# Performance work log

Measured on AMD Instinct MI355X. Metric: run time of the kernel, lower is better.

## Reference

```python
import jax, jax.numpy as jnp
import numpy as np

NPOINT = 2048
RADIUS = 0.1
NSAMPLE = 32


def fps(xyz, npoint):
    # Furthest point sampling, deterministic start at index 0 (matches pointnet2_utils).
    B, N, _ = xyz.shape
    dist0 = jnp.full((B, N), 1e10, dtype=xyz.dtype)
    far0 = jnp.zeros((B,), dtype=jnp.int32)

    def step(carry, _):
        dist, far = carry
        centroid = jnp.take_along_axis(xyz, far[:, None, None], axis=1)  # (B,1,3)
        d = jnp.sum((xyz - centroid) ** 2, axis=-1)                      # (B,N)
        dist = jnp.minimum(dist, d)
        new_far = jnp.argmax(dist, axis=-1).astype(jnp.int32)
        return (dist, new_far), far

    _, idx = jax.lax.scan(step, (dist0, far0), None, length=npoint)
    return idx.T  # (B, npoint)


def ball_query(xyz, new_xyz, radius, nsample):
    # For each center, indices of up to nsample points within radius (pad with first hit).
    N = xyz.shape[1]
    sqr = jnp.sum((new_xyz[:, :, None, :] - xyz[:, None, :, :]) ** 2, axis=-1)  # (B,S,N)
    cand = jnp.where(sqr <= radius * radius, jnp.arange(N, dtype=jnp.int32), N)
    cand = jnp.sort(cand, axis=-1)[:, :, :nsample]  # (B,S,K)
    first = cand[:, :, :1]
    first = jnp.where(first == N, 0, first)
    return jnp.where(cand == N, first, cand)


def batched_gather(points, idx):
    # points (B,N,C), idx (B,...) -> (B,...,C)
    return jax.vmap(lambda p, i: p[i])(points, idx)


def reference(xyz, features, W0, b0, W1, b1, W2, b2):
    # xyz: (B,N,3), features: (B,C,N)
    fps_idx = fps(xyz, NPOINT)                                  # (B,S)
    new_xyz = batched_gather(xyz, fps_idx)                      # (B,S,3)
    idx = ball_query(xyz, new_xyz, RADIUS, NSAMPLE)             # (B,S,K)

    grouped_xyz = batched_gather(xyz, idx) - new_xyz[:, :, None, :]   # (B,S,K,3) relative coords
    grouped_feat = batched_gather(features.transpose(0, 2, 1), idx)   # (B,S,K,C)
    grouped = jnp.concatenate([grouped_xyz, grouped_feat], axis=-1)   # (B,S,K,C+3)
    x = grouped.transpose(0, 3, 1, 2)                                 # (B,C+3,S,K)

    # SharedMLP: 1x1 conv2d + ReLU stack
    x = jax.nn.relu(jnp.einsum('oi,bisk->bosk', W0, x) + b0[None, :, None, None])
    x = jax.nn.relu(jnp.einsum('oi,bisk->bosk', W1, x) + b1[None, :, None, None])
    x = jax.nn.relu(jnp.einsum('oi,bisk->bosk', W2, x) + b2[None, :, None, None])

    new_features = jnp.max(x, axis=-1)  # max-pool over nsample -> (B,128,S)
    return new_xyz, new_features


def setup_inputs() -> dict:
    key = jax.random.key(0)
    ks = jax.random.split(key, 8)
    B, N, C = 4, 8192, 64
    s = 0.05  # keep activations in a sane range through 3 relu layers
    return {
        'xyz': jax.random.uniform(ks[0], (B, N, 3), dtype=jnp.float32),
        'features': jax.random.normal(ks[1], (B, C, N), dtype=jnp.float32),
        'W0': jax.random.normal(ks[2], (64, 67), dtype=jnp.float32) * s,
        'b0': jax.random.normal(ks[3], (64,), dtype=jnp.float32) * s,
        'W1': jax.random.normal(ks[4], (64, 64), dtype=jnp.float32) * s,
        'b1': jax.random.normal(ks[5], (64,), dtype=jnp.float32) * s,
        'W2': jax.random.normal(ks[6], (128, 64), dtype=jnp.float32) * s,
        'b2': jax.random.normal(ks[7], (128,), dtype=jnp.float32) * s,
    }
```

## Files before the change

kernel.cpp:

```cpp
#include <hip/hip_runtime.h>

#define NB 4
#define NPTS 8192
#define NPOINT 2048
#define NSAMPLE 32
#define CF 64
#define CIN 67
#define G 8

typedef float f32x2 __attribute__((ext_vector_type(2)));
typedef unsigned long long u64;

__device__ __forceinline__ f32x2 pk_add(f32x2 a, f32x2 b) {
  f32x2 d;
  asm("v_pk_add_f32 %0, %1, %2" : "=v"(d) : "v"(a), "v"(b));
  return d;
}
__device__ __forceinline__ f32x2 pk_mul(f32x2 a, f32x2 b) {
  f32x2 d;
  asm("v_pk_mul_f32 %0, %1, %2" : "=v"(d) : "v"(a), "v"(b));
  return d;
}

template <int CTRL, int RM>
__device__ __forceinline__ int dppi(int v) {
  return __builtin_amdgcn_update_dpp(0, v, CTRL, RM, 0xf, true);
}
template <int CTRL, int RM>
__device__ __forceinline__ u64 kstep(u64 k) {
  unsigned lo = (unsigned)k, hi = (unsigned)(k >> 32);
  unsigned olo = (unsigned)dppi<CTRL, RM>((int)lo);
  unsigned ohi = (unsigned)dppi<CTRL, RM>((int)hi);
  u64 o = ((u64)ohi << 32) | olo;
  return o > k ? o : k;
}

__global__ __launch_bounds__(512) void fps_kernel(const float* __restrict__ xyz,
                                                  float* __restrict__ new_xyz) {
  const int b = blockIdx.x;
  const int tid = threadIdx.x;
  __shared__ float sx[NPTS], sy[NPTS], sz[NPTS];
  __shared__ __align__(16) float cbuf[NPOINT * 3];
  __shared__ __align__(16) u64 skey[2][8];
  const float* xb = xyz + (size_t)b * NPTS * 3;
  for (int i = tid; i < NPTS; i += 512) {
    sx[i] = xb[3 * i + 0];
    sy[i] = xb[3 * i + 1];
    sz[i] = xb[3 * i + 2];
  }
  __syncthreads();
  f32x2 px[8], py[8], pz[8];
  float dist[16];
#pragma unroll
  for (int j = 0; j < 8; ++j) {
    int p0 = tid + (2 * j) * 512, p1 = tid + (2 * j + 1) * 512;
    px[j].x = sx[p0]; px[j].y = sx[p1];
    py[j].x = sy[p0]; py[j].y = sy[p1];
    pz[j].x = sz[p0]; pz[j].y = sz[p1];
    dist[2 * j] = 1e10f; dist[2 * j + 1] = 1e10f;
  }
  const int lane = tid & 63;
  const int wid = tid >> 6;
  int far = 0;
  for (int it = 0; it < NPOINT; ++it) {
    const float cx = sx[far], cy = sy[far], cz = sz[far];
    if (tid == 0) {
      cbuf[it * 3 + 0] = cx; cbuf[it * 3 + 1] = cy; cbuf[it * 3 + 2] = cz;
    }
    f32x2 ncx, ncy, ncz;
    ncx.x = -cx; ncx.y = -cx;
    ncy.x = -cy; ncy.y = -cy;
    ncz.x = -cz; ncz.y = -cz;
    float tb = -1.0f;
    int br = 0;
#pragma unroll
    for (int j = 0; j < 8; ++j) {
      f32x2 dx = pk_add(px[j], ncx);
      f32x2 dy = pk_add(py[j], ncy);
      f32x2 dz = pk_add(pz[j], ncz);
      f32x2 xx = pk_mul(dx, dx);
      f32x2 yy = pk_mul(dy, dy);
      f32x2 dd = pk_add(pk_add(xx, yy), pk_mul(dz, dz));
      float n0 = fminf(dist[2 * j], dd.x);
      float n1 = fminf(dist[2 * j + 1], dd.y);
      dist[2 * j] = n0; dist[2 * j + 1] = n1;
      bool g0 = n0 > tb; tb = g0 ? n0 : tb; br = g0 ? (2 * j) : br;
      bool g1 = n1 > tb; tb = g1 ? n1 : tb; br = g1 ? (2 * j + 1) : br;
    }
    u64 key = ((u64)__float_as_uint(tb) << 32) |
              (unsigned)~(unsigned)(tid + (br << 9));
    key = kstep<0x111, 0xf>(key);
    key = kstep<0x112, 0xf>(key);
    key = kstep<0x114, 0xf>(key);
    key = kstep<0x118, 0xf>(key);
    key = kstep<0x142, 0xa>(key);
    key = kstep<0x143, 0xc>(key);
    const int p = it & 1;
    if (lane == 63) skey[p][wid] = key;
    __syncthreads();
    const ulonglong2* kp = (const ulonglong2*)&skey[p][0];
    ulonglong2 k0 = kp[0], k1 = kp[1], k2 = kp[2], k3 = kp[3];
    u64 m0 = k0.x > k0.y ? k0.x : k0.y;
    u64 m1 = k1.x > k1.y ? k1.x : k1.y;
    u64 m2 = k2.x > k2.y ? k2.x : k2.y;
    u64 m3 = k3.x > k3.y ? k3.x : k3.y;
    u64 m4 = m0 > m1 ? m0 : m1;
    u64 m5 = m2 > m3 ? m2 : m3;
    u64 best = m4 > m5 ? m4 : m5;
    far = (int)~(unsigned)best;
  }
  __syncthreads();
  const float4* cb4 = (const float4*)cbuf;
  float4* o4 = (float4*)(new_xyz + (size_t)b * NPOINT * 3);
  for (int i = tid; i < NPOINT * 3 / 4; i += 512) o4[i] = cb4[i];
}

__global__ __launch_bounds__(256) void tr_kernel(const float* __restrict__ f,
                                                 float* __restrict__ ft) {
  int idx = blockIdx.x * 256 + threadIdx.x;
  int c = idx & 63;
  int i = (idx >> 6) & (NPTS - 1);
  int b = idx >> 19;
  ft[idx] = f[((size_t)(b * CF + c)) * NPTS + i];
}

__global__ __launch_bounds__(256) void bq_kernel(const float* __restrict__ xyz,
                                                 const float* __restrict__ new_xyz,
                                                 int* __restrict__ idxbuf) {
  const int lane = threadIdx.x & 63;
  const int gw = (blockIdx.x * 256 + threadIdx.x) >> 6;
  const int b = gw >> 11;
  const int j = gw & 2047;
  const float* xb = xyz + (size_t)b * NPTS * 3;
  const float* c = new_xyz + ((size_t)b * NPOINT + j) * 3;
  const float cx = c[0], cy = c[1], cz = c[2];
  int* out = idxbuf + ((size_t)b * NPOINT + j) * NSAMPLE;
  const float r2 = 0.01f;
  int found = 0, first = 0;
  for (int base = 0; base < NPTS && found < NSAMPLE; base += 64) {
    const int i = base + lane;
    float dx = xb[3 * i + 0] - cx, dy = xb[3 * i + 1] - cy, dz = xb[3 * i + 2] - cz;
    float d = __fadd_rn(__fadd_rn(__fmul_rn(dx, dx), __fmul_rn(dy, dy)),
                        __fmul_rn(dz, dz));
    bool in = (d <= r2);
    unsigned long long mask = __ballot(in);
    if (mask) {
      if (found == 0) first = base + (__ffsll(mask) - 1);
      int slot = found + __popcll(mask & ((1ull << lane) - 1ull));
      if (in && slot < NSAMPLE) out[slot] = i;
      found += (int)__popcll(mask);
    }
  }
  for (int s = found + lane; s < NSAMPLE; s += 64) out[s] = first;
}

__global__ __launch_bounds__(256) void mlp_kernel(const float* __restrict__ xyz,
                                                  const float* __restrict__ ft,
                                                  const float* __restrict__ feat,
                                                  const int* __restrict__ idxbuf,
                                                  const float* __restrict__ new_xyz,
                                                  const float* __restrict__ W0,
                                                  const float* __restrict__ b0,
                                                  const float* __restrict__ W1,
                                                  const float* __restrict__ b1,
                                                  const float* __restrict__ W2,
                                                  const float* __restrict__ b2,
                                                  float* __restrict__ out_nf,
                                                  int use_ft) {
  __shared__ __align__(16) float Ws0[CIN * 64];
  __shared__ __align__(16) float Ws1[64 * 64];
  __shared__ __align__(16) float Ws2[64 * 128];
  __shared__ float bs0[64], bs1[64], bs2[128];
  __shared__ __align__(16) float X0[CIN * 32];
  __shared__ __align__(16) float X1[64 * 32];
  const int tid = threadIdx.x;
  const int k = tid & 31;
  const int og = tid >> 5;
  for (int t = tid; t < 64 * CIN; t += 256) {
    int o = t / CIN, c = t - o * CIN;
    Ws0[c * 64 + o] = W0[t];
  }
  for (int t = tid; t < 64 * 64; t += 256) Ws1[(t & 63) * 64 + (t >> 6)] = W1[t];
  for (int t = tid; t < 128 * 64; t += 256) Ws2[(t & 63) * 128 + (t >> 6)] = W2[t];
  if (tid < 64) { bs0[tid] = b0[tid]; bs1[tid] = b1[tid]; }
  if (tid < 128) bs2[tid] = b2[tid];
  __syncthreads();

  for (int g = 0; g < G; ++g) {
    const int cj = blockIdx.x * G + g;
    const int b = cj >> 11;
    const int j = cj & 2047;
    const int ni = idxbuf[cj * NSAMPLE + k];
    if (og == 0) {
      const float* ctr = new_xyz + (size_t)cj * 3;
      const float* pp = xyz + ((size_t)b * NPTS + ni) * 3;
      X0[0 * 32 + k] = pp[0] - ctr[0];
      X0[1 * 32 + k] = pp[1] - ctr[1];
      X0[2 * 32 + k] = pp[2] - ctr[2];
    }
    const int cbase = 3 + og * 8;
    if (use_ft) {
      const float4* fr = (const float4*)(ft + ((size_t)b * NPTS + ni) * CF + og * 8);
      float4 f0 = fr[0], f1 = fr[1];
      X0[(cbase + 0) * 32 + k] = f0.x; X0[(cbase + 1) * 32 + k] = f0.y;
      X0[(cbase + 2) * 32 + k] = f0.z; X0[(cbase + 3) * 32 + k] = f0.w;
      X0[(cbase + 4) * 32 + k] = f1.x; X0[(cbase + 5) * 32 + k] = f1.y;
      X0[(cbase + 6) * 32 + k] = f1.z; X0[(cbase + 7) * 32 + k] = f1.w;
    } else {
      const float* fb = feat + (size_t)b * CF * NPTS + ni;
#pragma unroll
      for (int q = 0; q < 8; ++q)
        X0[(cbase + q) * 32 + k] = fb[(size_t)(og * 8 + q) * NPTS];
    }
    __syncthreads();

    float acc[8];
#pragma unroll
    for (int i = 0; i < 8; ++i) acc[i] = bs0[og * 8 + i];
    for (int c = 0; c < CIN; ++c) {
      float xv = X0[c * 32 + k];
      const float4* wr = (const float4*)&Ws0[c * 64 + og * 8];
      float4 w0 = wr[0], w1 = wr[1];
      acc[0] = fmaf(w0.x, xv, acc[0]); acc[1] = fmaf(w0.y, xv, acc[1]);
      acc[2] = fmaf(w0.z, xv, acc[2]); acc[3] = fmaf(w0.w, xv, acc[3]);
      acc[4] = fmaf(w1.x, xv, acc[4]); acc[5] = fmaf(w1.y, xv, acc[5]);
      acc[6] = fmaf(w1.z, xv, acc[6]); acc[7] = fmaf(w1.w, xv, acc[7]);
    }
#pragma unroll
    for (int i = 0; i < 8; ++i) X1[(og * 8 + i) * 32 + k] = fmaxf(acc[i], 0.f);
    __syncthreads();

    float a1[8];
#pragma unroll
    for (int i = 0; i < 8; ++i) a1[i] = bs1[og * 8 + i];
    for (int c = 0; c < 64; ++c) {
      float xv = X1[c * 32 + k];
      const float4* wr = (const float4*)&Ws1[c * 64 + og * 8];
      float4 w0 = wr[0], w1 = wr[1];
      a1[0] = fmaf(w0.x, xv, a1[0]); a1[1] = fmaf(w0.y, xv, a1[1]);
      a1[2] = fmaf(w0.z, xv, a1[2]); a1[3] = fmaf(w0.w, xv, a1[3]);
      a1[4] = fmaf(w1.x, xv, a1[4]); a1[5] = fmaf(w1.y, xv, a1[5]);
      a1[6] = fmaf(w1.z, xv, a1[6]); a1[7] = fmaf(w1.w, xv, a1[7]);
    }
#pragma unroll
    for (int i = 0; i < 8; ++i) X0[(og * 8 + i) * 32 + k] = fmaxf(a1[i], 0.f);
    __syncthreads();

    float a2[16];
#pragma unroll
    for (int i = 0; i < 16; ++i) a2[i] = bs2[og * 16 + i];
    for (int c = 0; c < 64; ++c) {
      float xv = X0[c * 32 + k];
      const float4* wr = (const float4*)&Ws2[c * 128 + og * 16];
      float4 w0 = wr[0], w1 = wr[1], w2 = wr[2], w3 = wr[3];
      a2[0]  = fmaf(w0.x, xv, a2[0]);  a2[1]  = fmaf(w0.y, xv, a2[1]);
      a2[2]  = fmaf(w0.z, xv, a2[2]);  a2[3]  = fmaf(w0.w, xv, a2[3]);
      a2[4]  = fmaf(w1.x, xv, a2[4]);  a2[5]  = fmaf(w1.y, xv, a2[5]);
      a2[6]  = fmaf(w1.z, xv, a2[6]);  a2[7]  = fmaf(w1.w, xv, a2[7]);
      a2[8]  = fmaf(w2.x, xv, a2[8]);  a2[9]  = fmaf(w2.y, xv, a2[9]);
      a2[10] = fmaf(w2.z, xv, a2[10]); a2[11] = fmaf(w2.w, xv, a2[11]);
      a2[12] = fmaf(w3.x, xv, a2[12]); a2[13] = fmaf(w3.y, xv, a2[13]);
      a2[14] = fmaf(w3.z, xv, a2[14]); a2[15] = fmaf(w3.w, xv, a2[15]);
    }
#pragma unroll
    for (int i = 0; i < 16; ++i) {
      float v = fmaxf(a2[i], 0.f);
#pragma unroll
      for (int m = 1; m < 32; m <<= 1) v = fmaxf(v, __shfl_xor(v, m));
      a2[i] = v;
    }
    if (k == 0) {
#pragma unroll
      for (int i = 0; i < 16; ++i)
        out_nf[((size_t)b * 128 + og * 16 + i) * NPOINT + j] = a2[i];
    }
    __syncthreads();
  }
}

extern "C" void kernel_launch(void* const* d_in, const int* in_sizes, int n_in,
                              void* d_out, int out_size, void* d_ws, size_t ws_size,
                              hipStream_t stream) {
  (void)in_sizes; (void)n_in; (void)out_size;
  const float* xyz  = (const float*)d_in[0];
  const float* feat = (const float*)d_in[1];
  const float* W0   = (const float*)d_in[2];
  const float* b0   = (const float*)d_in[3];
  const float* W1   = (const float*)d_in[4];
  const float* b1   = (const float*)d_in[5];
  const float* W2   = (const float*)d_in[6];
  const float* b2   = (const float*)d_in[7];
  float* new_xyz = (float*)d_out;
  float* out_nf  = (float*)d_out + (size_t)NB * NPOINT * 3;

  int* idxbuf = (int*)d_ws;
  size_t idx_bytes = (size_t)NB * NPOINT * NSAMPLE * sizeof(int);
  float* ft = (float*)((char*)d_ws + idx_bytes);
  size_t need = idx_bytes + (size_t)NB * NPTS * CF * sizeof(float);
  int use_ft = (ws_size >= need) ? 1 : 0;

  fps_kernel<<<NB, 512, 0, stream>>>(xyz, new_xyz);
  if (use_ft) tr_kernel<<<(NB * NPTS * CF) / 256, 256, 0, stream>>>(feat, ft);
  bq_kernel<<<(NB * NPOINT) / 4, 256, 0, stream>>>(xyz, new_xyz, idxbuf);
  mlp_kernel<<<(NB * NPOINT) / G, 256, 0, stream>>>(xyz, ft, feat, idxbuf, new_xyz,
                                                    W0, b0, W1, b1, W2, b2,
                                                    out_nf, use_ft);
}
```

Measured before the change: 2.319 ms.

## Sort FPS points by Morton cell and skip distance updates via bounding-box bound

Before the FPS loop, points are bucketed into an 8x8x8 Morton-ordered grid with shared-memory counting sort, so each thread owns 16 spatially nearby points and tracks their bounding box. On each iteration a thread skips its distance update when the box's minimum distance to the new centroid cannot lower its current maximum, reusing its cached key. The aim is to cut the per-iteration ALU work of the serial FPS loop. It adds setup cost, an extra argmax key encoding by original index (tie-break kept), and wave divergence; the barrier and reduction per iteration remain.

Result: faster. 2.133 ms (-8.0%).

```diff
diff --git a/kernel.cpp b/kernel.cpp
--- a/kernel.cpp
+++ b/kernel.cpp
@@ -34,67 +34,142 @@
   u64 o = ((u64)ohi << 32) | olo;
   return o > k ? o : k;
 }
+__device__ __forceinline__ u64 wave_max_key(u64 key) {
+  key = kstep<0x111, 0xf>(key);
+  key = kstep<0x112, 0xf>(key);
+  key = kstep<0x114, 0xf>(key);
+  key = kstep<0x118, 0xf>(key);
+  key = kstep<0x142, 0xa>(key);
+  key = kstep<0x143, 0xc>(key);
+  return key;
+}
+__device__ __forceinline__ unsigned wave_scan_incl(unsigned v) {
+  v += (unsigned)__builtin_amdgcn_update_dpp(0, (int)v, 0x111, 0xf, 0xf, true);
+  v += (unsigned)__builtin_amdgcn_update_dpp(0, (int)v, 0x112, 0xf, 0xf, true);
+  v += (unsigned)__builtin_amdgcn_update_dpp(0, (int)v, 0x114, 0xf, 0xf, true);
+  v += (unsigned)__builtin_amdgcn_update_dpp(0, (int)v, 0x118, 0xf, 0xf, true);
+  v += (unsigned)__builtin_amdgcn_update_dpp(0, (int)v, 0x142, 0xa, 0xf, true);
+  v += (unsigned)__builtin_amdgcn_update_dpp(0, (int)v, 0x143, 0xc, 0xf, true);
+  return v;
+}
+
+__device__ __forceinline__ int cellof(float x) {
+  int c = (int)(x * 8.0f);
+  return c > 7 ? 7 : (c < 0 ? 0 : c);
+}
+__device__ __forceinline__ unsigned morton9(int ix, int iy, int iz) {
+  unsigned m = 0;
+#pragma unroll
+  for (int k = 0; k < 3; ++k) {
+    m |= ((unsigned)((ix >> k) & 1) << (3 * k + 2)) |
+         ((unsigned)((iy >> k) & 1) << (3 * k + 1)) |
+         ((unsigned)((iz >> k) & 1) << (3 * k + 0));
+  }
+  return m;
+}
 
 __global__ __launch_bounds__(512) void fps_kernel(const float* __restrict__ xyz,
                                                   float* __restrict__ new_xyz) {
   const int b = blockIdx.x;
   const int tid = threadIdx.x;
+  const int lane = tid & 63;
+  const int wid = tid >> 6;
   __shared__ float sx[NPTS], sy[NPTS], sz[NPTS];
-  __shared__ __align__(16) float cbuf[NPOINT * 3];
+  __shared__ unsigned sidx[NPTS];
+  __shared__ unsigned offs[512];
+  __shared__ unsigned wsum[8];
+  __shared__ int farhist[NPOINT];
   __shared__ __align__(16) u64 skey[2][8];
+
   const float* xb = xyz + (size_t)b * NPTS * 3;
   for (int i = tid; i < NPTS; i += 512) {
     sx[i] = xb[3 * i + 0];
     sy[i] = xb[3 * i + 1];
     sz[i] = xb[3 * i + 2];
   }
-  __syncthreads();
+  offs[tid] = 0;
+  __syncthreads();
+  for (int r = 0; r < 16; ++r) {
+    int i = tid + r * 512;
+    unsigned m = morton9(cellof(sx[i]), cellof(sy[i]), cellof(sz[i]));
+    atomicAdd(&offs[m], 1u);
+  }
+  __syncthreads();
+  unsigned v = offs[tid];
+  unsigned inc = wave_scan_incl(v);
+  if (lane == 63) wsum[wid] = inc;
+  __syncthreads();
+  unsigned pre = 0;
+#pragma unroll
+  for (int w = 0; w < 8; ++w) pre += (w < wid) ? wsum[w] : 0u;
+  unsigned excl = pre + inc - v;
+  __syncthreads();
+  offs[tid] = excl;
+  __syncthreads();
+  for (int r = 0; r < 16; ++r) {
+    int i = tid + r * 512;
+    unsigned m = morton9(cellof(sx[i]), cellof(sy[i]), cellof(sz[i]));
+    unsigned pos = atomicAdd(&offs[m], 1u);
+    sidx[pos] = (unsigned)i;
+  }
+  __syncthreads();
+
   f32x2 px[8], py[8], pz[8];
   float dist[16];
+  unsigned noid[16];
+  float blx = 1e30f, bhx = -1e30f, bly = 1e30f, bhy = -1e30f,
+        blz = 1e30f, bhz = -1e30f;
 #pragma unroll
   for (int j = 0; j < 8; ++j) {
-    int p0 = tid + (2 * j) * 512, p1 = tid + (2 * j + 1) * 512;
-    px[j].x = sx[p0]; px[j].y = sx[p1];
-    py[j].x = sy[p0]; py[j].y = sy[p1];
-    pz[j].x = sz[p0]; pz[j].y = sz[p1];
+    unsigned i0 = sidx[tid * 16 + 2 * j], i1 = sidx[tid * 16 + 2 * j + 1];
+    noid[2 * j] = ~i0; noid[2 * j + 1] = ~i1;
+    float x0 = sx[i0], x1 = sx[i1];
+    float y0 = sy[i0], y1 = sy[i1];
+    float z0 = sz[i0], z1 = sz[i1];
+    px[j].x = x0; px[j].y = x1;
+    py[j].x = y0; py[j].y = y1;
+    pz[j].x = z0; pz[j].y = z1;
+    blx = fminf(blx, fminf(x0, x1)); bhx = fmaxf(bhx, fmaxf(x0, x1));
+    bly = fminf(bly, fminf(y0, y1)); bhy = fmaxf(bhy, fmaxf(y0, y1));
+    blz = fminf(blz, fminf(z0, z1)); bhz = fmaxf(bhz, fmaxf(z0, z1));
     dist[2 * j] = 1e10f; dist[2 * j + 1] = 1e10f;
   }
-  const int lane = tid & 63;
-  const int wid = tid >> 6;
+  float gmaxd = 1e30f;
+  u64 gkey = 0;
   int far = 0;
   for (int it = 0; it < NPOINT; ++it) {
+    if (tid == 0) farhist[it] = far;
     const float cx = sx[far], cy = sy[far], cz = sz[far];
-    if (tid == 0) {
-      cbuf[it * 3 + 0] = cx; cbuf[it * 3 + 1] = cy; cbuf[it * 3 + 2] = cz;
-    }
-    f32x2 ncx, ncy, ncz;
-    ncx.x = -cx; ncx.y = -cx;
-    ncy.x = -cy; ncy.y = -cy;
-    ncz.x = -cz; ncz.y = -cz;
-    float tb = -1.0f;
-    int br = 0;
-#pragma unroll
-    for (int j = 0; j < 8; ++j) {
-      f32x2 dx = pk_add(px[j], ncx);
-      f32x2 dy = pk_add(py[j], ncy);
-      f32x2 dz = pk_add(pz[j], ncz);
-      f32x2 xx = pk_mul(dx, dx);
-      f32x2 yy = pk_mul(dy, dy);
-      f32x2 dd = pk_add(pk_add(xx, yy), pk_mul(dz, dz));
-      float n0 = fminf(dist[2 * j], dd.x);
-      float n1 = fminf(dist[2 * j + 1], dd.y);
-      dist[2 * j] = n0; dist[2 * j + 1] = n1;
-      bool g0 = n0 > tb; tb = g0 ? n0 : tb; br = g0 ? (2 * j) : br;
-      bool g1 = n1 > tb; tb = g1 ? n1 : tb; br = g1 ? (2 * j + 1) : br;
-    }
-    u64 key = ((u64)__float_as_uint(tb) << 32) |
-              (unsigned)~(unsigned)(tid + (br << 9));
-    key = kstep<0x111, 0xf>(key);
-    key = kstep<0x112, 0xf>(key);
-    key = kstep<0x114, 0xf>(key);
-    key = kstep<0x118, 0xf>(key);
-    key = kstep<0x142, 0xa>(key);
-    key = kstep<0x143, 0xc>(key);
+    float gx = fmaxf(fmaxf(blx - cx, cx - bhx), 0.f);
+    float gy = fmaxf(fmaxf(bly - cy, cy - bhy), 0.f);
+    float gz = fmaxf(fmaxf(blz - cz, cz - bhz), 0.f);
+    float mind2 = gx * gx + gy * gy + gz * gz;
+    if (mind2 * 0.999f < gmaxd) {
+      f32x2 ncx, ncy, ncz;
+      ncx.x = -cx; ncx.y = -cx;
+      ncy.x = -cy; ncy.y = -cy;
+      ncz.x = -cz; ncz.y = -cz;
+      u64 k = 0;
+#pragma unroll
+      for (int j = 0; j < 8; ++j) {
+        f32x2 dx = pk_add(px[j], ncx);
+        f32x2 dy = pk_add(py[j], ncy);
+        f32x2 dz = pk_add(pz[j], ncz);
+        f32x2 xx = pk_mul(dx, dx);
+        f32x2 yy = pk_mul(dy, dy);
+        f32x2 dd = pk_add(pk_add(xx, yy), pk_mul(dz, dz));
+        float n0 = fminf(dist[2 * j], dd.x);
+        float n1 = fminf(dist[2 * j + 1], dd.y);
+        dist[2 * j] = n0; dist[2 * j + 1] = n1;
+        u64 k0 = ((u64)__float_as_uint(n0) << 32) | noid[2 * j];
+        k = k0 > k ? k0 : k;
+        u64 k1 = ((u64)__float_as_uint(n1) << 32) | noid[2 * j + 1];
+        k = k1 > k ? k1 : k;
+      }
+      gkey = k;
+      gmaxd = __uint_as_float((unsigned)(k >> 32));
+    }
+    u64 key = wave_max_key(gkey);
     const int p = it & 1;
     if (lane == 63) skey[p][wid] = key;
     __syncthreads();
@@ -110,9 +185,11 @@
     far = (int)~(unsigned)best;
   }
   __syncthreads();
-  const float4* cb4 = (const float4*)cbuf;
-  float4* o4 = (float4*)(new_xyz + (size_t)b * NPOINT * 3);
-  for (int i = tid; i < NPOINT * 3 / 4; i += 512) o4[i] = cb4[i];
+  for (int t = tid; t < NPOINT; t += 512) {
+    int f = farhist[t];
+    float* o = new_xyz + ((size_t)b * NPOINT + t) * 3;
+    o[0] = sx[f]; o[1] = sy[f]; o[2] = sz[f];
+  }
 }
 
 __global__ __launch_bounds__(256) void tr_kernel(const float* __restrict__ f,
```
